# Kernel optimization log

Measured on AMD Instinct MI355X. Metric: run time of the kernel, lower is better.

## Reference

```python
import jax, jax.numpy as jnp
import numpy as np
from jax import lax

V = 32000   # vocab_size
H = 1024    # hidden_size
B = 32      # batch
S = 64      # encoder (source) length
T = 64      # decoder (target) length


def setup_inputs() -> dict:
    key = jax.random.key(0)
    ks = jax.random.split(key, 16)
    scale = 0.05

    def p(k, shape):
        return jax.random.normal(k, shape, dtype=jnp.float32) * scale

    input_seqs = jax.random.randint(ks[0], (B, S), 0, V)
    target_seqs = jax.random.randint(ks[1], (B, T), 0, V)
    # pack_padded_sequence requires descending-sorted lengths >= 1
    input_lens = jnp.sort(jax.random.randint(ks[2], (B,), S // 2, S + 1))[::-1].astype(jnp.int32)

    return {
        "input_seqs": input_seqs,
        "target_seqs": target_seqs,
        "input_lens": input_lens,
        # encoder params (torch GRU layout: gates [r|z|n] stacked on first dim)
        "emb_enc": p(ks[3], (V, H)),
        "W_ih_e": p(ks[4], (3 * H, H)),
        "W_hh_e": p(ks[5], (3 * H, H)),
        "b_ih_e": p(ks[6], (3 * H,)),
        "b_hh_e": p(ks[7], (3 * H,)),
        # decoder params (GRU input size is 2H due to [embedded ; thought] concat)
        "emb_dec": p(ks[8], (V, H)),
        "W_ih_d": p(ks[9], (3 * H, 2 * H)),
        "W_hh_d": p(ks[10], (3 * H, H)),
        "b_ih_d": p(ks[11], (3 * H,)),
        "b_hh_d": p(ks[12], (3 * H,)),
        "W_out": p(ks[13], (V, H)),
        "b_out": p(ks[14], (V,)),
    }


def _gru_step(xp_t, h, W_hh, b_hh):
    """One torch-style GRU step. xp_t = x_t @ W_ih.T + b_ih, shape [B, 3H]."""
    gh = h @ W_hh.T + b_hh                     # [B, 3H]
    xr, xz, xn = jnp.split(xp_t, 3, axis=-1)
    hr, hz, hn = jnp.split(gh, 3, axis=-1)
    r = jax.nn.sigmoid(xr + hr)
    z = jax.nn.sigmoid(xz + hz)
    n = jnp.tanh(xn + r * hn)
    return (1.0 - z) * n + z * h


def reference(input_seqs, target_seqs, input_lens,
              emb_enc, W_ih_e, W_hh_e, b_ih_e, b_hh_e,
              emb_dec, W_ih_d, W_hh_d, b_ih_d, b_hh_d,
              W_out, b_out):
    b, s = input_seqs.shape
    t = target_seqs.shape[1]
    h_dim = emb_enc.shape[1]

    # ---------------- Encoder (packed GRU == masked recurrence) ----------------
    x = emb_enc[input_seqs]                                   # [B, S, H]
    xp = jnp.einsum('bsh,gh->bsg', x, W_ih_e) + b_ih_e        # [B, S, 3H], all input projs at once
    valid = jnp.arange(s)[:, None] < input_lens[None, :]      # [S, B]

    def enc_step(h, inp):
        xp_t, m_t = inp                                       # [B,3H], [B]
        h_new = _gru_step(xp_t, h, W_hh_e, b_hh_e)
        # packed sequence: hidden frozen past each row's true length
        return jnp.where(m_t[:, None], h_new, h), None

    h0 = jnp.zeros((b, h_dim), dtype=x.dtype)
    thought, _ = lax.scan(enc_step, h0, (xp.transpose(1, 0, 2), valid))  # [B, H]

    # ---------------- Decoder ----------------
    e = emb_dec[target_seqs]                                  # [B, T, H]
    # create_rnn_input: broadcast-concat thought onto every timestep
    rnn_in = jnp.concatenate(
        [e, jnp.broadcast_to(thought[:, None, :], (b, t, h_dim))], axis=-1)  # [B, T, 2H]
    rnn_in = jax.nn.relu(rnn_in)                              # F.relu before the GRU
    xp_d = jnp.einsum('bsh,gh->bsg', rnn_in, W_ih_d) + b_ih_d # [B, T, 3H]

    def dec_step(h, xp_t):
        h_new = _gru_step(xp_t, h, W_hh_d, b_hh_d)
        return h_new, h_new

    h0d = jnp.zeros((b, h_dim), dtype=e.dtype)                # decoder init_hidden = zeros
    _, hs = lax.scan(dec_step, h0d, xp_d.transpose(1, 0, 2))  # [T, B, H]

    logits = jnp.einsum('tbh,vh->tbv', hs, W_out) + b_out     # [T, B, V]
    log_probs = jax.nn.log_softmax(logits, axis=-1)           # softmax_batch == per-row log_softmax
    return log_probs.transpose(1, 0, 2)                       # [B, T, V]
```

## Files before the change

### kernel.cpp

```cpp
#include <hip/hip_runtime.h>
#include <stdint.h>
#include <stddef.h>

#define VOCAB 32000
#define HID   1024
#define NB    32
#define SLEN  64
#define TLEN  64
#define G3    3072

typedef float          f32x4  __attribute__((ext_vector_type(4)));
typedef float          f32x2  __attribute__((ext_vector_type(2)));
typedef __bf16         bf16x8 __attribute__((ext_vector_type(8)));
typedef unsigned short u16x8  __attribute__((ext_vector_type(8)));
typedef unsigned short u16x4  __attribute__((ext_vector_type(4)));
typedef unsigned int   u32x4  __attribute__((ext_vector_type(4)));

union BfPun { u16x8 u; bf16x8 b; };
union CvPun { u32x4 u; bf16x8 b; };

__device__ __forceinline__ unsigned short f2bf(float f) {
  unsigned int u = __builtin_bit_cast(unsigned int, f);
  u += 0x7FFFu + ((u >> 16) & 1u);
  return (unsigned short)(u >> 16);
}

__device__ __forceinline__ float sig_f(float x) {
  return __builtin_amdgcn_rcpf(1.f + __expf(-x));
}
__device__ __forceinline__ float tanh_f(float x) {
  return 2.f * __builtin_amdgcn_rcpf(1.f + __expf(-2.f * x)) - 1.f;
}

__device__ __forceinline__ void gld_lds16(const unsigned short* g, unsigned short* l) {
  __builtin_amdgcn_global_load_lds(
      (const __attribute__((address_space(1))) unsigned int*)g,
      (__attribute__((address_space(3))) unsigned int*)l,
      16, 0, 0);
}


__global__ __launch_bounds__(256) void cvt_bf16(const float* __restrict__ in,
                                                unsigned short* __restrict__ out) {
  size_t idx = ((size_t)blockIdx.x * 256 + threadIdx.x) * 4;
  f32x4 v = *(const f32x4*)(in + idx);
  u16x4 o;
  o[0] = f2bf(v[0]); o[1] = f2bf(v[1]); o[2] = f2bf(v[2]); o[3] = f2bf(v[3]);
  *(u16x4*)(out + idx) = o;
}

__global__ __launch_bounds__(256) void cvt_split_d(const float* __restrict__ Wd,
                                                   unsigned short* __restrict__ W1,
                                                   unsigned short* __restrict__ W2) {
  int r = blockIdx.x, q = threadIdx.x;
  const float* src = Wd + (size_t)r * 2048;
  f32x4 v1 = *(const f32x4*)(src + q * 4);
  f32x4 v2 = *(const f32x4*)(src + 1024 + q * 4);
  u16x4 o1, o2;
  o1[0]=f2bf(v1[0]); o1[1]=f2bf(v1[1]); o1[2]=f2bf(v1[2]); o1[3]=f2bf(v1[3]);
  o2[0]=f2bf(v2[0]); o2[1]=f2bf(v2[1]); o2[2]=f2bf(v2[2]); o2[3]=f2bf(v2[3]);
  *(u16x4*)(W1 + (size_t)r * 1024 + q * 4) = o1;
  *(u16x4*)(W2 + (size_t)r * 1024 + q * 4) = o2;
}

__global__ __launch_bounds__(128) void cvt_whh_frag(const float* __restrict__ W,
                                                    unsigned short* __restrict__ Wv) {
  int r = blockIdx.x;
  int g = r >> 10, i = r & 1023, blk = i >> 4, il = i & 15;
  int q = threadIdx.x;
  int ks = q >> 2, ksub = q & 3, lane = il + ksub * 16;
  f32x4 v0 = *(const f32x4*)(W + (size_t)r * HID + q * 8);
  f32x4 v1 = *(const f32x4*)(W + (size_t)r * HID + q * 8 + 4);
  u16x8 o;
  o[0]=f2bf(v0[0]); o[1]=f2bf(v0[1]); o[2]=f2bf(v0[2]); o[3]=f2bf(v0[3]);
  o[4]=f2bf(v1[0]); o[5]=f2bf(v1[1]); o[6]=f2bf(v1[2]); o[7]=f2bf(v1[3]);
  size_t dst = ((((size_t)blk * 3 + g) * 32 + ks) * 64 + lane) * 8;
  *(u16x8*)(Wv + dst) = o;
}

__global__ __launch_bounds__(256) void gather_embed(const int* __restrict__ seqs,
                                                    const float* __restrict__ emb,
                                                    unsigned short* __restrict__ Aout,
                                                    int relu) {
  int r = blockIdx.x, q = threadIdx.x;
  int tok = seqs[r];
  f32x4 v = *(const f32x4*)(emb + (size_t)tok * HID + q * 4);
  if (relu) {
    v[0]=fmaxf(v[0],0.f); v[1]=fmaxf(v[1],0.f); v[2]=fmaxf(v[2],0.f); v[3]=fmaxf(v[3],0.f);
  }
  u16x4 o; o[0]=f2bf(v[0]); o[1]=f2bf(v[1]); o[2]=f2bf(v[2]); o[3]=f2bf(v[3]);
  *(u16x4*)(Aout + (size_t)r * HID + q * 4) = o;
}

__global__ __launch_bounds__(256) void gather_thought(const float* __restrict__ hfin,
                                                      unsigned short* __restrict__ Aout) {
  int r = blockIdx.x, q = threadIdx.x;
  u16x4 o = {0, 0, 0, 0};
  if (r < NB) {
    f32x4 v = *(const f32x4*)(hfin + (size_t)r * HID + q * 4);
    o[0]=f2bf(fmaxf(v[0],0.f)); o[1]=f2bf(fmaxf(v[1],0.f));
    o[2]=f2bf(fmaxf(v[2],0.f)); o[3]=f2bf(fmaxf(v[3],0.f));
  }
  *(u16x4*)(Aout + (size_t)r * HID + q * 4) = o;
}

__global__ __launch_bounds__(256) void zero_f32(float* __restrict__ p) {
  p[blockIdx.x * 256 + threadIdx.x] = 0.f;
}

template<int MODE, int MT>
__global__ __launch_bounds__(256) void gemm_bf16(const unsigned short* __restrict__ A,
                                                 const unsigned short* __restrict__ Bw,
                                                 const float* __restrict__ bias,
                                                 const float* __restrict__ add2,
                                                 float* __restrict__ out, int N) {
  __shared__ unsigned short Abuf[128 * 32];
  __shared__ unsigned short Bbuf[128 * 32];
  const int K = HID;
  int tid = threadIdx.x, lane = tid & 63, wid = tid >> 6;
  int nwg = gridDim.x;
  int u = (blockIdx.x & 7) * (nwg >> 3) + (blockIdx.x >> 3);
  int g = u / (MT * 4);
  int r_ = u - g * (MT * 4);
  int bm = r_ % MT;
  int bn = g * 4 + r_ / MT;
  int wrow = wid >> 1, wcol = wid & 1;
  f32x4 zero4 = {0.f, 0.f, 0.f, 0.f};
  f32x4 acc[4][4];
#pragma unroll
  for (int i = 0; i < 4; ++i)
#pragma unroll
    for (int j = 0; j < 4; ++j) acc[i][j] = zero4;

  int srow = tid >> 2, spart = tid & 3;
  const unsigned short* Ag = A + ((size_t)bm * 128 + srow) * K + spart * 8;
  const unsigned short* Bg = Bw + ((size_t)bn * 128 + srow) * K + spart * 8;
  unsigned short* As = Abuf + tid * 8;
  unsigned short* Bs = Bbuf + tid * 8;

  for (int ks = 0; ks < 32; ++ks) {
    int k0 = ks * 32;
    __syncthreads();
    gld_lds16(Ag + k0, As);
    gld_lds16(Ag + (size_t)64 * K + k0, As + 64 * 32);
    gld_lds16(Bg + k0, Bs);
    gld_lds16(Bg + (size_t)64 * K + k0, Bs + 64 * 32);
    __syncthreads();
    bf16x8 af[4], bfr[4];
#pragma unroll
    for (int mi = 0; mi < 4; ++mi) {
      BfPun tpun;
      tpun.u = *(const u16x8*)(Abuf + (wrow * 64 + mi * 16 + (lane & 15)) * 32 + (lane >> 4) * 8);
      af[mi] = tpun.b;
    }
#pragma unroll
    for (int ni = 0; ni < 4; ++ni) {
      BfPun tpun;
      tpun.u = *(const u16x8*)(Bbuf + (wcol * 64 + ni * 16 + (lane & 15)) * 32 + (lane >> 4) * 8);
      bfr[ni] = tpun.b;
    }
#pragma unroll
    for (int mi = 0; mi < 4; ++mi)
#pragma unroll
      for (int ni = 0; ni < 4; ++ni)
        acc[mi][ni] = __builtin_amdgcn_mfma_f32_16x16x32_bf16(af[mi], bfr[ni], acc[mi][ni], 0, 0, 0);
  }

#pragma unroll
  for (int mi = 0; mi < 4; ++mi) {
    int rb = bm * 128 + wrow * 64 + mi * 16 + ((lane >> 4) << 2);
#pragma unroll
    for (int ni = 0; ni < 4; ++ni) {
      int c = bn * 128 + wcol * 64 + ni * 16 + (lane & 15);
#pragma unroll
      for (int e = 0; e < 4; ++e) {
        int r = rb + e;
        float v = acc[mi][ni][e];
        if (MODE == 0) {
          out[(size_t)r * N + c] = v + bias[c];
        } else if (MODE == 1) {
          int t = r & 63, b = r >> 6;
          int gg = c >> 10, ci = c & 1023;
          out[(((size_t)t * 3 + gg) * NB + b) * HID + ci] = v + bias[c];
        } else if (MODE == 2) {
          int t = r & 63, b = r >> 6;
          int gg = c >> 10, ci = c & 1023;
          out[(((size_t)t * 3 + gg) * NB + b) * HID + ci] = v + add2[(size_t)b * G3 + c];
        } else {
          int b = r & 31, t = r >> 5;
          out[((size_t)b * TLEN + t) * VOCAB + c] = v + bias[c];
        }
      }
    }
  }
}

__global__ __launch_bounds__(384, 1) void gru_scan(
    const unsigned short* __restrict__ Wv,
    const float* __restrict__ b_hh,
    const float* __restrict__ xpT,
    unsigned short* __restrict__ hbx,
    const int* __restrict__ lens,
    unsigned short* __restrict__ hs_out,
    float* __restrict__ hfin,
    int* __restrict__ bar, int nsteps) {
  __shared__ unsigned short Wlds[49152];
  __shared__ float gh[48][33];
  __shared__ float h32[32][16];
  __shared__ float bhh_s[48];
  __shared__ int   lens_s[32];
  int tid = threadIdx.x, lane = tid & 63, w = tid >> 6;
  int g = w >> 1, part = w & 1;
  int blk = blockIdx.x, i0 = blk * 16;

  if (tid < 32) lens_s[tid] = lens ? lens[tid] : 0x7fffffff;
  if (tid >= 64 && tid < 112) {
    int q = tid - 64;
    bhh_s[q] = b_hh[(size_t)(q >> 4) * HID + i0 + (q & 15)];
  }
  if (tid < 256) h32[tid >> 3][((tid & 7) * 2)] = 0.f;
  if (tid < 256) h32[tid >> 3][((tid & 7) * 2) + 1] = 0.f;

  {
    const unsigned short* Wsrc = Wv + (size_t)blk * 49152;
    for (int j = tid; j < 6144; j += 384)
      *(u16x8*)(Wlds + (size_t)j * 8) = *(const u16x8*)(Wsrc + (size_t)j * 8);
  }
  __syncthreads();

  int eb = tid >> 3, eil = (tid & 7) * 2;
  f32x2 xr2, xz2, xn2;

  for (int t = 0; t < nsteps; ++t) {
    if (tid < 256) {
      const float* xb = xpT + ((size_t)t * 3 * NB + eb) * HID + i0 + eil;
      xr2 = *(const f32x2*)(xb);
      xz2 = *(const f32x2*)(xb + (size_t)NB * HID);
      xn2 = *(const f32x2*)(xb + (size_t)2 * NB * HID);
    }
    f32x4 acc = {0.f, 0.f, 0.f, 0.f};
    if (t > 0) {
      const unsigned short* hp = hbx + (size_t)(t - 1) * 32768 + part * 16384 + lane * 8;
      u32x4 pb[16];
#pragma unroll
      for (int j = 0; j < 16; ++j) pb[j] = *(const u32x4*)(hp + (size_t)j * 512);
#pragma unroll
      for (int ks = 0; ks < 32; ++ks) {
        BfPun a_;
        a_.u = *(const u16x8*)(Wlds + ((size_t)(g * 32 + ks) * 64 + lane) * 8);
        CvPun cv; cv.u = pb[ks & 15];
        if (ks + 16 < 32) pb[ks & 15] = *(const u32x4*)(hp + (size_t)(ks + 16) * 512);
        acc = __builtin_amdgcn_mfma_f32_16x16x32_bf16(a_.b, cv.b, acc, 0, 0, 0);
      }
    }
    {
      int il4 = (lane >> 4) * 4, cb = part * 16 + (lane & 15);
#pragma unroll
      for (int e = 0; e < 4; ++e) gh[g * 16 + il4 + e][cb] = acc[e];
    }
    __syncthreads();

    if (tid < 256) {
      float sr0 = gh[eil][eb],      sr1 = gh[eil + 1][eb];
      float sz0 = gh[16 + eil][eb], sz1 = gh[16 + eil + 1][eb];
      float sn0 = gh[32 + eil][eb], sn1 = gh[32 + eil + 1][eb];
      float rg0 = sig_f(xr2[0] + sr0 + bhh_s[eil]);
      float rg1 = sig_f(xr2[1] + sr1 + bhh_s[eil + 1]);
      float zg0 = sig_f(xz2[0] + sz0 + bhh_s[16 + eil]);
      float zg1 = sig_f(xz2[1] + sz1 + bhh_s[16 + eil + 1]);
      float ng0 = tanh_f(xn2[0] + rg0 * (sn0 + bhh_s[32 + eil]));
      float ng1 = tanh_f(xn2[1] + rg1 * (sn1 + bhh_s[32 + eil + 1]));
      float h0o = h32[eb][eil], h1o = h32[eb][eil + 1];
      float hn0 = (1.f - zg0) * ng0 + zg0 * h0o;
      float hn1 = (1.f - zg1) * ng1 + zg1 * h1o;
      if (t >= lens_s[eb]) { hn0 = h0o; hn1 = h1o; }
      h32[eb][eil] = hn0; h32[eb][eil + 1] = hn1;
      unsigned int pk = (unsigned int)f2bf(hn0) | ((unsigned int)f2bf(hn1) << 16);
      int k = i0 + eil;
      int ksf = k >> 5, lnf = (eb & 15) + ((k >> 3) & 3) * 16, sub = k & 7;
      unsigned short* dst = hbx + (size_t)t * 32768 + (size_t)(eb >> 4) * 16384
                            + (size_t)ksf * 512 + lnf * 8 + sub;
      __hip_atomic_store((unsigned int*)dst, pk, __ATOMIC_RELAXED, __HIP_MEMORY_SCOPE_AGENT);
      if (hs_out)
        *(unsigned int*)(hs_out + ((size_t)t * NB + eb) * HID + k) = pk;
    }

    if (t + 1 < nsteps) {
      __syncthreads();
      if (tid == 0)
        __hip_atomic_fetch_add(&bar[(t * 8 + (blk & 7)) * 16], 1,
                               __ATOMIC_RELAXED, __HIP_MEMORY_SCOPE_AGENT);
      if (tid < 64) {
        const int* cp = &bar[(t * 8 + (lane & 7)) * 16];
        while (__hip_atomic_load(cp, __ATOMIC_RELAXED, __HIP_MEMORY_SCOPE_AGENT) < 8)
          __builtin_amdgcn_s_sleep(1);
      }
      __syncthreads();
    }
  }

  if (hfin && tid < 256) {
    f32x2 hv; hv[0] = h32[eb][eil]; hv[1] = h32[eb][eil + 1];
    *(f32x2*)(hfin + (size_t)eb * HID + i0 + eil) = hv;
  }
}

__global__ __launch_bounds__(1024, 1) void log_softmax_lds(float* __restrict__ out) {
  __shared__ float rowbuf[VOCAB];
  __shared__ float ms[16], ss[16];
  size_t row = blockIdx.x;
  float* p = out + row * VOCAB;
  const f32x4* p4 = (const f32x4*)p;
  int tid = threadIdx.x;
  float m = -3.0e38f, s = 0.f;
  for (int j = tid; j < VOCAB / 4; j += 1024) {
    f32x4 v = p4[j];
    *(f32x4*)(rowbuf + j * 4) = v;
#pragma unroll
    for (int e = 0; e < 4; ++e) {
      float x = v[e];
      float nm = fmaxf(m, x);
      s = s * __expf(m - nm) + __expf(x - nm);
      m = nm;
    }
  }
#pragma unroll
  for (int off = 1; off < 64; off <<= 1) {
    float m2 = __shfl_xor(m, off, 64);
    float s2 = __shfl_xor(s, off, 64);
    float nm = fmaxf(m, m2);
    s = s * __expf(m - nm) + s2 * __expf(m2 - nm);
    m = nm;
  }
  if ((tid & 63) == 0) { ms[tid >> 6] = m; ss[tid >> 6] = s; }
  __syncthreads();
  float M = -3.0e38f;
#pragma unroll
  for (int i = 0; i < 16; ++i) M = fmaxf(M, ms[i]);
  float S = 0.f;
#pragma unroll
  for (int i = 0; i < 16; ++i) S += ss[i] * __expf(ms[i] - M);
  float lse = M + __logf(S);
  f32x4* o4 = (f32x4*)p;
  for (int j = tid; j < VOCAB / 4; j += 1024) {
    f32x4 v = *(const f32x4*)(rowbuf + j * 4);
    v[0] -= lse; v[1] -= lse; v[2] -= lse; v[3] -= lse;
    o4[j] = v;
  }
}


extern "C" void kernel_launch(void* const* d_in, const int* in_sizes, int n_in,
                              void* d_out, int out_size, void* d_ws, size_t ws_size,
                              hipStream_t stream) {
  (void)in_sizes; (void)n_in; (void)out_size; (void)ws_size;
  const int*   input_seqs  = (const int*)d_in[0];
  const int*   target_seqs = (const int*)d_in[1];
  const int*   input_lens  = (const int*)d_in[2];
  const float* emb_enc = (const float*)d_in[3];
  const float* W_ih_e  = (const float*)d_in[4];
  const float* W_hh_e  = (const float*)d_in[5];
  const float* b_ih_e  = (const float*)d_in[6];
  const float* b_hh_e  = (const float*)d_in[7];
  const float* emb_dec = (const float*)d_in[8];
  const float* W_ih_d  = (const float*)d_in[9];
  const float* W_hh_d  = (const float*)d_in[10];
  const float* b_ih_d  = (const float*)d_in[11];
  const float* b_hh_d  = (const float*)d_in[12];
  const float* W_out   = (const float*)d_in[13];
  const float* b_out   = (const float*)d_in[14];
  float* out = (float*)d_out;

  char* p = (char*)d_ws;
  auto take = [&](size_t n) { char* q = p; p += (n + 255) & ~(size_t)255; return q; };
  unsigned short* Wbf_e  = (unsigned short*)take((size_t)G3 * HID * 2);
  unsigned short* Wbf_1d = (unsigned short*)take((size_t)G3 * HID * 2);
  unsigned short* Wbf_2d = (unsigned short*)take((size_t)G3 * HID * 2);
  unsigned short* Wbf_o  = (unsigned short*)take((size_t)VOCAB * HID * 2);
  unsigned short* Wv_e   = (unsigned short*)take((size_t)G3 * HID * 2);
  unsigned short* Wv_d   = (unsigned short*)take((size_t)G3 * HID * 2);
  unsigned short* A_ed   = (unsigned short*)take((size_t)2048 * HID * 2);
  unsigned short* A_th   = (unsigned short*)take((size_t)128 * HID * 2);
  unsigned short* A_hs   = (unsigned short*)take((size_t)2048 * HID * 2);
  float* xpT = (float*)take((size_t)64 * 3 * NB * HID * 4);
  float* t2  = (float*)take((size_t)128 * G3 * 4);
  unsigned short* hbx_e = (unsigned short*)take((size_t)SLEN * NB * HID * 2);
  unsigned short* hbx_d = (unsigned short*)take((size_t)TLEN * NB * HID * 2);
  int*   bar_e = (int*)take((size_t)SLEN * 8 * 16 * 4);
  int*   bar_d = (int*)take((size_t)TLEN * 8 * 16 * 4);
  float* hfin = (float*)take((size_t)NB * HID * 4);

  cvt_bf16<<<dim3((G3 * HID) / 1024), 256, 0, stream>>>(W_ih_e, Wbf_e);
  cvt_split_d<<<dim3(G3), 256, 0, stream>>>(W_ih_d, Wbf_1d, Wbf_2d);
  cvt_bf16<<<dim3((VOCAB * HID) / 1024), 256, 0, stream>>>(W_out, Wbf_o);
  cvt_whh_frag<<<dim3(G3), 128, 0, stream>>>(W_hh_e, Wv_e);
  cvt_whh_frag<<<dim3(G3), 128, 0, stream>>>(W_hh_d, Wv_d);
  zero_f32<<<dim3(64), 256, 0, stream>>>((float*)bar_e);

  gather_embed<<<dim3(NB * SLEN), 256, 0, stream>>>(input_seqs, emb_enc, A_ed, 0);
  gemm_bf16<1, 16><<<dim3(384), 256, 0, stream>>>(A_ed, Wbf_e, b_ih_e, nullptr, xpT, G3);
  gru_scan<<<dim3(64), 384, 0, stream>>>(Wv_e, b_hh_e, xpT, hbx_e, input_lens,
                                         nullptr, hfin, bar_e, SLEN);

  gather_thought<<<dim3(128), 256, 0, stream>>>(hfin, A_th);
  gemm_bf16<0, 1><<<dim3(24), 256, 0, stream>>>(A_th, Wbf_2d, b_ih_d, nullptr, t2, G3);
  gather_embed<<<dim3(NB * TLEN), 256, 0, stream>>>(target_seqs, emb_dec, A_ed, 1);
  gemm_bf16<2, 16><<<dim3(384), 256, 0, stream>>>(A_ed, Wbf_1d, nullptr, t2, xpT, G3);

  gru_scan<<<dim3(64), 384, 0, stream>>>(Wv_d, b_hh_d, xpT, hbx_d, nullptr,
                                         A_hs, nullptr, bar_d, TLEN);

  gemm_bf16<3, 16><<<dim3(4000), 256, 0, stream>>>(A_hs, Wbf_o, b_out, nullptr, out, VOCAB);
  log_softmax_lds<<<dim3(NB * TLEN), 1024, 0, stream>>>(out);
}
```

Measured before the change: 892.4 us.

## Deepen GEMM K-tile with XOR-swizzled LDS and store logits as bf16

The GEMM now stages a 64-wide K slice per iteration instead of 32, which halves the barrier count, and applies an XOR swizzle to the LDS layout to avoid bank conflicts. The output-projection GEMM writes bf16 logits into the first half of each fp32 output row, and the log-softmax kernel reads those bf16 values back, which halves the intermediate write and read traffic. The cost is that logits are rounded to bf16 before the log-softmax, which loses precision. The in-place trick relies on each row's bf16 data being read into LDS before that row's fp32 results overwrite it.

```diff
diff --git a/kernel.cpp b/kernel.cpp
--- a/kernel.cpp
+++ b/kernel.cpp
@@ -23,6 +23,10 @@
   unsigned int u = __builtin_bit_cast(unsigned int, f);
   u += 0x7FFFu + ((u >> 16) & 1u);
   return (unsigned short)(u >> 16);
+}
+__device__ __forceinline__ float bf2f(unsigned short h) {
+  unsigned int u = (unsigned int)h << 16;
+  return __builtin_bit_cast(float, u);
 }
 
 __device__ __forceinline__ float sig_f(float x) {
@@ -113,9 +117,9 @@
                                                  const unsigned short* __restrict__ Bw,
                                                  const float* __restrict__ bias,
                                                  const float* __restrict__ add2,
-                                                 float* __restrict__ out, int N) {
-  __shared__ unsigned short Abuf[128 * 32];
-  __shared__ unsigned short Bbuf[128 * 32];
+                                                 void* __restrict__ outv, int N) {
+  __shared__ unsigned short Abuf[128 * 64];
+  __shared__ unsigned short Bbuf[128 * 64];
   const int K = HID;
   int tid = threadIdx.x, lane = tid & 63, wid = tid >> 6;
   int nwg = gridDim.x;
@@ -132,40 +136,52 @@
 #pragma unroll
     for (int j = 0; j < 4; ++j) acc[i][j] = zero4;
 
-  int srow = tid >> 2, spart = tid & 3;
-  const unsigned short* Ag = A + ((size_t)bm * 128 + srow) * K + spart * 8;
-  const unsigned short* Bg = Bw + ((size_t)bn * 128 + srow) * K + spart * 8;
+  int srow = tid >> 3;
+  int csrc = (tid & 7) ^ (srow & 7);
+  const unsigned short* Ag = A + ((size_t)bm * 128 + srow) * K + csrc * 8;
+  const unsigned short* Bg = Bw + ((size_t)bn * 128 + srow) * K + csrc * 8;
   unsigned short* As = Abuf + tid * 8;
   unsigned short* Bs = Bbuf + tid * 8;
 
-  for (int ks = 0; ks < 32; ++ks) {
-    int k0 = ks * 32;
+  int ca0 = (0 * 4 + (lane >> 4)) ^ (lane & 7);
+  int ca1 = (1 * 4 + (lane >> 4)) ^ (lane & 7);
+
+  for (int ks = 0; ks < 16; ++ks) {
+    size_t k0 = ks * 64;
     __syncthreads();
-    gld_lds16(Ag + k0, As);
-    gld_lds16(Ag + (size_t)64 * K + k0, As + 64 * 32);
-    gld_lds16(Bg + k0, Bs);
-    gld_lds16(Bg + (size_t)64 * K + k0, Bs + 64 * 32);
+#pragma unroll
+    for (int j = 0; j < 4; ++j)
+      gld_lds16(Ag + (size_t)j * 32 * K + k0, As + j * 2048);
+#pragma unroll
+    for (int j = 0; j < 4; ++j)
+      gld_lds16(Bg + (size_t)j * 32 * K + k0, Bs + j * 2048);
     __syncthreads();
-    bf16x8 af[4], bfr[4];
-#pragma unroll
-    for (int mi = 0; mi < 4; ++mi) {
-      BfPun tpun;
-      tpun.u = *(const u16x8*)(Abuf + (wrow * 64 + mi * 16 + (lane & 15)) * 32 + (lane >> 4) * 8);
-      af[mi] = tpun.b;
-    }
-#pragma unroll
-    for (int ni = 0; ni < 4; ++ni) {
-      BfPun tpun;
-      tpun.u = *(const u16x8*)(Bbuf + (wcol * 64 + ni * 16 + (lane & 15)) * 32 + (lane >> 4) * 8);
-      bfr[ni] = tpun.b;
-    }
-#pragma unroll
-    for (int mi = 0; mi < 4; ++mi)
-#pragma unroll
-      for (int ni = 0; ni < 4; ++ni)
-        acc[mi][ni] = __builtin_amdgcn_mfma_f32_16x16x32_bf16(af[mi], bfr[ni], acc[mi][ni], 0, 0, 0);
-  }
-
+#pragma unroll
+    for (int kk = 0; kk < 2; ++kk) {
+      int cc = kk ? ca1 : ca0;
+      bf16x8 af[4], bfr[4];
+#pragma unroll
+      for (int mi = 0; mi < 4; ++mi) {
+        BfPun tpun;
+        tpun.u = *(const u16x8*)(Abuf + (wrow * 64 + mi * 16 + (lane & 15)) * 64 + cc * 8);
+        af[mi] = tpun.b;
+      }
+#pragma unroll
+      for (int ni = 0; ni < 4; ++ni) {
+        BfPun tpun;
+        tpun.u = *(const u16x8*)(Bbuf + (wcol * 64 + ni * 16 + (lane & 15)) * 64 + cc * 8);
+        bfr[ni] = tpun.b;
+      }
+#pragma unroll
+      for (int mi = 0; mi < 4; ++mi)
+#pragma unroll
+        for (int ni = 0; ni < 4; ++ni)
+          acc[mi][ni] = __builtin_amdgcn_mfma_f32_16x16x32_bf16(af[mi], bfr[ni], acc[mi][ni], 0, 0, 0);
+    }
+  }
+
+  float* out = (float*)outv;
+  unsigned short* o16 = (unsigned short*)outv;
 #pragma unroll
   for (int mi = 0; mi < 4; ++mi) {
     int rb = bm * 128 + wrow * 64 + mi * 16 + ((lane >> 4) << 2);
@@ -188,7 +204,7 @@
           out[(((size_t)t * 3 + gg) * NB + b) * HID + ci] = v + add2[(size_t)b * G3 + c];
         } else {
           int b = r & 31, t = r >> 5;
-          out[((size_t)b * TLEN + t) * VOCAB + c] = v + bias[c];
+          o16[(size_t)(b * 64 + t) * (VOCAB * 2) + c] = f2bf(v + bias[c]);
         }
       }
     }
@@ -305,20 +321,19 @@
   }
 }
 
-__global__ __launch_bounds__(1024, 1) void log_softmax_lds(float* __restrict__ out) {
+__global__ __launch_bounds__(1024, 1) void log_softmax_bf16(float* __restrict__ out) {
   __shared__ float rowbuf[VOCAB];
   __shared__ float ms[16], ss[16];
   size_t row = blockIdx.x;
-  float* p = out + row * VOCAB;
-  const f32x4* p4 = (const f32x4*)p;
+  const unsigned short* src = (const unsigned short*)out + row * (VOCAB * 2);
   int tid = threadIdx.x;
   float m = -3.0e38f, s = 0.f;
-  for (int j = tid; j < VOCAB / 4; j += 1024) {
-    f32x4 v = p4[j];
-    *(f32x4*)(rowbuf + j * 4) = v;
-#pragma unroll
-    for (int e = 0; e < 4; ++e) {
-      float x = v[e];
+  for (int j = tid; j < VOCAB / 8; j += 1024) {
+    u16x8 v = *(const u16x8*)(src + j * 8);
+#pragma unroll
+    for (int e = 0; e < 8; ++e) {
+      float x = bf2f(v[e]);
+      rowbuf[j * 8 + e] = x;
       float nm = fmaxf(m, x);
       s = s * __expf(m - nm) + __expf(x - nm);
       m = nm;
@@ -341,7 +356,7 @@
 #pragma unroll
   for (int i = 0; i < 16; ++i) S += ss[i] * __expf(ms[i] - M);
   float lse = M + __logf(S);
-  f32x4* o4 = (f32x4*)p;
+  f32x4* o4 = (f32x4*)(out + row * VOCAB);
   for (int j = tid; j < VOCAB / 4; j += 1024) {
     f32x4 v = *(const f32x4*)(rowbuf + j * 4);
     v[0] -= lse; v[1] -= lse; v[2] -= lse; v[3] -= lse;
@@ -411,5 +426,5 @@
                                          A_hs, nullptr, bar_d, TLEN);
 
   gemm_bf16<3, 16><<<dim3(4000), 256, 0, stream>>>(A_hs, Wbf_o, b_out, nullptr, out, VOCAB);
-  log_softmax_lds<<<dim3(NB * TLEN), 1024, 0, stream>>>(out);
-}
+  log_softmax_bf16<<<dim3(NB * TLEN), 1024, 0, stream>>>(out);
+}
```

Result: faster. 870.4 us (-2.5%).
